# Kernel optimization log

Hardware: AMD Instinct MI355X
Metric: run time of the kernel (lower is better)

## Reference

```python
import jax, jax.numpy as jnp
import numpy as np
from functools import partial

V, H, B, T, L = 32000, 1024, 64, 64, 4
EOS = 2


def setup_inputs() -> dict:
    key = jax.random.key(0)
    ks = jax.random.split(key, 10)
    s = 1.0 / np.sqrt(H)
    return {
        "max_len": T,
        "tgt": jax.random.randint(ks[0], (B, T), 0, V),
        "h0": jax.random.normal(ks[1], (L, B, H), jnp.float32),
        "c0": jax.random.normal(ks[2], (L, B, H), jnp.float32),
        "embedding": jax.random.normal(ks[3], (V, H), jnp.float32) * s,
        "W_ih": jax.random.normal(ks[4], (L, 4 * H, H), jnp.float32) * s,
        "W_hh": jax.random.normal(ks[5], (L, 4 * H, H), jnp.float32) * s,
        "b_ih": jax.random.normal(ks[6], (L, 4 * H), jnp.float32) * s,
        "b_hh": jax.random.normal(ks[7], (L, 4 * H), jnp.float32) * s,
        "W_cls": jax.random.normal(ks[8], (V, H), jnp.float32) * s,
        "b_cls": jax.random.normal(ks[9], (V,), jnp.float32) * s,
    }


def _lstm_cell(x, h, c, Wi, Wh, bi, bh):
    # gates: [B, 4H] in torch order (i, f, g, o)
    g = x @ Wi.T + bi + h @ Wh.T + bh
    i, f, gg, o = jnp.split(g, 4, axis=-1)
    c2 = jax.nn.sigmoid(f) * c + jax.nn.sigmoid(i) * jnp.tanh(gg)
    h2 = jax.nn.sigmoid(o) * jnp.tanh(c2)
    return h2, c2


def reference(max_len, tgt, h0, c0, embedding, W_ih, W_hh, b_ih, b_hh, W_cls, b_cls):
    # step i>0 uses embedding of tgt[:, i-1].
    batch = tgt.shape[0]
    x0 = jnp.broadcast_to(embedding[EOS], (batch, embedding.shape[1]))
    tf_in = embedding[tgt[:, : max_len - 1]]              # [B, T-1, H]
    inputs = jnp.concatenate([x0[:, None, :], tf_in], axis=1)  # [B, T, H]
    inputs = jnp.swapaxes(inputs, 0, 1)                   # [T, B, H]

    def step(carry, x):
        h, c = carry  # each [L, B, H]
        hs, cs = [], []
        inp = x
        for l in range(L):  # 4 stacked LSTM cells, h of cell l feeds cell l+1
            hn, cn = _lstm_cell(inp, h[l], c[l], W_ih[l], W_hh[l], b_ih[l], b_hh[l])
            hs.append(hn)
            cs.append(cn)
            inp = hn
        h = jnp.stack(hs)
        c = jnp.stack(cs)
        logp = jax.nn.log_softmax(h[L - 1] @ W_cls.T + b_cls, axis=-1)  # [B, V]
        return (h, c), logp

    (h, c), out = jax.lax.scan(step, (h0, c0), inputs)
    return out, h, c  # out: [T, B, V]
```

## Files before the change

kernel.cpp:

```cpp
#include <hip/hip_runtime.h>

using u16 = unsigned short;
using u32 = unsigned int;

typedef __bf16 bf16x8 __attribute__((ext_vector_type(8)));
typedef float  f32x4  __attribute__((ext_vector_type(4)));
typedef u16    u16x8  __attribute__((ext_vector_type(8)));

static constexpr int kV = 32000, kH = 1024, kB = 64, kT = 64, kL = 4, kEOS = 2;

struct Flag { int v; int pad[15]; };

__device__ __forceinline__ u16 f2bf(float f) {
  u32 u = __float_as_uint(f);
  u = (u + 0x7fffu + ((u >> 16) & 1u)) >> 16;
  return (u16)u;
}
__device__ __forceinline__ float sigf(float x)   { return 1.0f / (1.0f + __expf(-x)); }
__device__ __forceinline__ float tanhf_(float x) { return 1.0f - 2.0f / (__expf(2.0f * x) + 1.0f); }

typedef const __attribute__((address_space(1))) u32* gas_ptr;
typedef __attribute__((address_space(3))) u32*       las_ptr;
__device__ __forceinline__ void async16(const u16* g, u16* l) {
  __builtin_amdgcn_global_load_lds((gas_ptr)g, (las_ptr)l, 16, 0, 0);
}

__device__ __forceinline__ void spin_ge(const int* p, int tgt) {
  while (__hip_atomic_load(p, __ATOMIC_RELAXED, __HIP_MEMORY_SCOPE_AGENT) < tgt)
    __builtin_amdgcn_s_sleep(2);
}

__device__ __forceinline__ size_t packed_off(int b, int k) {
  return (size_t)(((b >> 4) * 32 + (k >> 5)) * 512 + (((k >> 3) & 3) * 16 + (b & 15)) * 8 + (k & 7));
}

__device__ __forceinline__ u16x8 cvt8(const float* src) {
  const float4* s4 = (const float4*)src;
  float4 v0 = s4[0], v1 = s4[1];
  u16x8 r;
  r[0]=f2bf(v0.x); r[1]=f2bf(v0.y); r[2]=f2bf(v0.z); r[3]=f2bf(v0.w);
  r[4]=f2bf(v1.x); r[5]=f2bf(v1.y); r[6]=f2bf(v1.z); r[7]=f2bf(v1.w);
  return r;
}


__global__ void __launch_bounds__(256)
pack_lstm(const float* __restrict__ Wih, const float* __restrict__ Whh,
          u16* __restrict__ wpack) {
  __shared__ u16 lds[64 * 136];
  const int bid = blockIdx.x;
  const int lblk = bid >> 4, mt = (bid >> 3) & 1, kkg = bid & 7;
  const int lay = lblk >> 6, cb = lblk & 63;
  const int tid = threadIdx.x;
  const float* W = mt ? Whh : Wih;
  {
    const int rid = tid >> 2, q = tid & 3;
    const int gr = (rid >> 4) * 1024 + cb * 16 + (rid & 15);
    const float* src = W + ((size_t)lay * 4096 + gr) * 1024 + kkg * 128 + q * 32;
    u16* dst = lds + rid * 136 + q * 32;
    #pragma unroll
    for (int it = 0; it < 4; ++it)
      *(u16x8*)(dst + it * 8) = cvt8(src + it * 8);
  }
  __syncthreads();
  const int cf = tid >> 6, lane = tid & 63;
  const int rid = cf * 16 + (lane & 15);
  const int l4o = (lane >> 4) * 8;
  #pragma unroll
  for (int kl = 0; kl < 4; ++kl) {
    const int kk = kkg * 4 + kl;
    const u16x8 v = *(const u16x8*)(lds + rid * 136 + kl * 32 + l4o);
    *(u16x8*)(wpack + ((size_t)lblk * 16384 + mt * 8192 + kk * 256 + cf * 64 + lane) * 8) = v;
  }
}

__global__ void __launch_bounds__(256)
pack_cls(const float* __restrict__ W, u16* __restrict__ o) {
  __shared__ u16 lds[128 * 136];
  const int bid = blockIdx.x;
  const int bn = bid >> 3, kkg = bid & 7;
  const int tid = threadIdx.x;
  {
    const int row = tid >> 1, half = tid & 1;
    const float* src = W + ((size_t)(bn * 128 + row)) * 1024 + kkg * 128 + half * 64;
    u16* dst = lds + row * 136 + half * 64;
    #pragma unroll
    for (int it = 0; it < 8; ++it)
      *(u16x8*)(dst + it * 8) = cvt8(src + it * 8);
  }
  __syncthreads();
  #pragma unroll
  for (int kl = 0; kl < 4; ++kl) {
    const int kk = kkg * 4 + kl;
    #pragma unroll
    for (int q = 0; q < 2; ++q) {
      const int p = tid + q * 256, row = p & 127, l4 = p >> 7;
      const u16x8 v = *(const u16x8*)(lds + row * 136 + kl * 32 + l4 * 8);
      *(u16x8*)(o + ((size_t)bn * 16384 + kk * 512 + p) * 8) = v;
    }
  }
}

__global__ void pack_x(const float* __restrict__ emb, const int* __restrict__ tgt,
                       u16* __restrict__ X) {
  const int cid = blockIdx.x * 256 + threadIdx.x;
  const int kc = cid & 127, b = (cid >> 7) & 63, t = cid >> 13;
  const int tok = (t == 0) ? kEOS : tgt[b * 64 + t - 1];
  const u16x8 r = cvt8(emb + (size_t)tok * 1024 + kc * 8);
  *(u16x8*)(X + (size_t)t * 65536 + packed_off(b, kc * 8)) = r;
}

__global__ void pack_init(const float* __restrict__ h0, const float* __restrict__ bih,
                          const float* __restrict__ bhh, u16* __restrict__ hball,
                          float* __restrict__ bsum) {
  const int cid = blockIdx.x * 256 + threadIdx.x;
  if (cid < 32768) {
    const int kc = cid & 127, row = cid >> 7;
    const int lay = row >> 6, b = row & 63;
    const u16x8 r = cvt8(h0 + (size_t)cid * 8);
    *(u16x8*)(hball + (size_t)lay * 65 * 65536 + packed_off(b, kc * 8)) = r;
  } else {
    const int i = cid - 32768;
    bsum[i] = bih[i] + bhh[i];
  }
}

__global__ void __launch_bounds__(1024, 4)
lstm_coop(const u16* __restrict__ wpack, const u16* __restrict__ xall,
          u16* __restrict__ hball, const float* __restrict__ bsum,
          const float* __restrict__ c0, float* __restrict__ outh, float* __restrict__ outc,
          Flag* flags) {
  __shared__ u16 stg[3][32][512];
  __shared__ float Gc[2][64][80];

  const int tid = threadIdx.x, lane = tid & 63, wave = tid >> 6;
  const int l15 = lane & 15, l4 = lane >> 4;
  const int cmat = wave >> 3, cwc = (wave >> 1) & 3, ckh = wave & 1;
  const int blk = blockIdx.x;
  const int lay = (blk >> 1) & 3;
  const int cb  = ((blk >> 3) << 1) | (blk & 1);
  const int u0 = cb << 4;
  const int ub = tid >> 4, uu = tid & 15;

  float creg = c0[((size_t)lay * 64 + ub) * 1024 + u0 + uu];
  float bsv[4];
  #pragma unroll
  for (int g = 0; g < 4; ++g) bsv[g] = bsum[lay * 4096 + g * 1024 + u0 + uu];

  const size_t wbase = (size_t)(lay * 64 + cb) * 131072;
  bf16x8 breg[16];
  #pragma unroll
  for (int j = 0; j < 16; ++j)
    breg[j] = *(const bf16x8*)(wpack + wbase
        + (size_t)(((cmat * 32 + 2 * j + ckh) * 4) + cwc) * 512 + lane * 8);

  const int j0 = wave * 2, j1 = wave * 2 + 1;
  const int m2a = j0 >> 4, mta = (j0 >> 2) & 3, ksla = j0 & 3;
  const int m2b = j1 >> 4, mtb = (j1 >> 2) & 3, kslb = j1 & 3;

  u16* hlay = hball + (size_t)lay * 65 * 65536;
  const u16* hprev = (lay == 0) ? xall : (hball + (size_t)(lay - 1) * 65 * 65536);

  #pragma unroll 1
  for (int t = 0; t < kT; ++t) {
    if (t > 0 && tid < 64)                 spin_ge(&flags[lay * 64 + tid].v, t);
    if (lay > 0 && tid >= 64 && tid < 128) spin_ge(&flags[(lay - 1) * 64 + (tid - 64)].v, t + 1);
    __syncthreads();

    const u16* xsrc = (lay == 0) ? (xall + (size_t)t * 65536)
                                 : (hprev + (size_t)(t + 1) * 65536);
    const u16* hsrc = hlay + (size_t)t * 65536;

    const u16* ga = (m2a ? hsrc : xsrc) + (size_t)((mta * 32 + ksla) * 512) + lane * 8;
    const u16* gb = (m2b ? hsrc : xsrc) + (size_t)((mtb * 32 + kslb) * 512) + lane * 8;

    auto STAGE = [&](int c) {
      async16(ga + (size_t)c * 2048, &stg[c % 3][m2a * 16 + mta * 4 + ksla][0]);
      async16(gb + (size_t)c * 2048, &stg[c % 3][m2b * 16 + mtb * 4 + kslb][0]);
    };

    f32x4 acc[4] = {};
    STAGE(0); STAGE(1);
    #pragma unroll
    for (int c = 0; c < 8; ++c) {
      if (c < 7) asm volatile("s_waitcnt vmcnt(2)" ::: "memory");
      else       asm volatile("s_waitcnt vmcnt(0)" ::: "memory");
      __builtin_amdgcn_s_barrier();
      asm volatile("" ::: "memory");
      if (c < 6) STAGE(c + 2);
      const u16* As = &stg[c % 3][cmat * 16][0];
      #pragma unroll
      for (int s = 0; s < 2; ++s) {
        const int ksl = 2 * s + ckh;
        bf16x8 a[4];
        #pragma unroll
        for (int m = 0; m < 4; ++m)
          a[m] = *(const bf16x8*)(As + (m * 4 + ksl) * 512 + lane * 8);
        #pragma unroll
        for (int m = 0; m < 4; ++m)
          acc[m] = __builtin_amdgcn_mfma_f32_16x16x32_bf16(a[m], breg[2 * c + s], acc[m], 0, 0, 0);
      }
    }

    if (ckh == 0) {
      #pragma unroll
      for (int m = 0; m < 4; ++m)
        #pragma unroll
        for (int r = 0; r < 4; ++r)
          Gc[cmat][m * 16 + l4 * 4 + r][cwc * 16 + l15] = acc[m][r];
    }
    __syncthreads();
    if (ckh == 1) {
      #pragma unroll
      for (int m = 0; m < 4; ++m)
        #pragma unroll
        for (int r = 0; r < 4; ++r)
          Gc[cmat][m * 16 + l4 * 4 + r][cwc * 16 + l15] += acc[m][r];
    }
    __syncthreads();

    float sg[4];
    #pragma unroll
    for (int g = 0; g < 4; ++g) {
      const int col = g * 16 + uu;
      sg[g] = Gc[0][ub][col] + Gc[1][ub][col] + bsv[g];
    }
    const float c2 = sigf(sg[1]) * creg + sigf(sg[0]) * tanhf_(sg[2]);
    const float h2 = sigf(sg[3]) * tanhf_(c2);
    creg = c2;
    const u16 hv = f2bf(h2);
    if (t == kT - 1) {
      outh[((size_t)lay * 64 + ub) * 1024 + u0 + uu] = h2;
      outc[((size_t)lay * 64 + ub) * 1024 + u0 + uu] = c2;
    }
    const u32 other = __shfl_xor((u32)hv, 1);
    if ((tid & 1) == 0) {
      const u32 hpair = (u32)hv | (other << 16);
      u32* hdst = (u32*)(hlay + (size_t)(t + 1) * 65536 + packed_off(ub, u0 + uu));
      __hip_atomic_store(hdst, hpair, __ATOMIC_RELAXED, __HIP_MEMORY_SCOPE_AGENT);
    }
    __syncthreads();
    if (tid == 0)
      __hip_atomic_store(&flags[lay * 64 + cb].v, t + 1, __ATOMIC_RELAXED, __HIP_MEMORY_SCOPE_AGENT);
  }
}

#define CLS_EPILOGUE()                                                                     \
  {                                                                                        \
    float* sRm = (float*)&sA[0][0];                                          \
    float* sRs = sRm + 256;                                                                \
    _Pragma("unroll")                                                                      \
    for (int mi = 0; mi < 4; ++mi) {                                                       \
      _Pragma("unroll")                                                                    \
      for (int r = 0; r < 4; ++r) {                                                        \
        float v[4];                                                                        \
        _Pragma("unroll")                                                                  \
        for (int ci = 0; ci < 4; ++ci) v[ci] = acc[mi][ci][r] + bc[ci];                     \
        float mx = fmaxf(fmaxf(v[0], v[1]), fmaxf(v[2], v[3]));                            \
        mx = fmaxf(mx, __shfl_xor(mx, 1)); mx = fmaxf(mx, __shfl_xor(mx, 2));              \
        mx = fmaxf(mx, __shfl_xor(mx, 4)); mx = fmaxf(mx, __shfl_xor(mx, 8));              \
        float ss = __expf(v[0]-mx) + __expf(v[1]-mx) + __expf(v[2]-mx) + __expf(v[3]-mx);  \
        ss += __shfl_xor(ss, 1); ss += __shfl_xor(ss, 2);                                  \
        ss += __shfl_xor(ss, 4); ss += __shfl_xor(ss, 8);                                  \
        const int lr = wm * 64 + mi * 16 + l4 * 4 + r;                                     \
        if (l15 == 0) { sRm[wc * 128 + lr] = mx; sRs[wc * 128 + lr] = ss; }                \
      }                                                                                    \
    }                                                                                      \
    __syncthreads();                                                                       \
    if (tid < 128) {                                                                       \
      const float m0 = sRm[tid], s0 = sRs[tid];                                            \
      const float m1 = sRm[128 + tid], s1 = sRs[128 + tid];                                \
      const float M = fmaxf(m0, m1);                                                       \
      const float S = s0 * __expf(m0 - M) + s1 * __expf(m1 - M);                           \
      pmax[(size_t)(bm * 128 + tid) * 256 + bn] = M;                                       \
      psum[(size_t)(bm * 128 + tid) * 256 + bn] = S;                                       \
    }                                                                                      \
  }

__global__ void __launch_bounds__(256)
cls_gemm(const u16* __restrict__ A, const u16* __restrict__ Bw,
         const float* __restrict__ bcls, float* __restrict__ out,
         float* __restrict__ pmax, float* __restrict__ psum) {
  __shared__ u16 sA[3][4096], sB[3][4096];
  const int tid = threadIdx.x, lane = tid & 63, wave = tid >> 6;
  const int wm = wave >> 1, wc = wave & 1;
  const int l15 = lane & 15, l4 = lane >> 4;
  const int bm = blockIdx.x, bn = blockIdx.y;
  const u16* Ab = A  + (size_t)bm * 131072;
  const u16* Bb = Bw + (size_t)bn * 131072;

  auto STAGE = [&](int kk) {
    u16* dA = sA[kk % 3]; u16* dB = sB[kk % 3];
    #pragma unroll
    for (int q = 0; q < 4; ++q) {
      const int u = wave * 4 + q;
      if (u < 8) {
        const u16* g = Ab + (size_t)(u >> 2) * 65536 + (size_t)(((u & 3) * 32 + kk) * 512) + lane * 8;
        async16(g, dA + u * 512);
      } else {
        const int v = u & 7;
        const u16* g = Bb + (size_t)kk * 4096 + v * 512 + lane * 8;
        async16(g, dB + v * 512);
      }
    }
  };

  f32x4 acc[4][4] = {};
  STAGE(0); STAGE(1);
  for (int kk = 0; kk < 32; ++kk) {
    if (kk < 31) asm volatile("s_waitcnt vmcnt(4)" ::: "memory");
    else         asm volatile("s_waitcnt vmcnt(0)" ::: "memory");
    __builtin_amdgcn_s_barrier();
    asm volatile("" ::: "memory");
    if (kk < 30) STAGE(kk + 2);
    const u16* aS = sA[kk % 3]; const u16* bS = sB[kk % 3];
    bf16x8 av[4], bv[4];
    #pragma unroll
    for (int mi = 0; mi < 4; ++mi) av[mi] = *(const bf16x8*)(aS + (wm * 4 + mi) * 512 + lane * 8);
    #pragma unroll
    for (int ci = 0; ci < 4; ++ci) bv[ci] = *(const bf16x8*)(bS + l4 * 1024 + (wc * 64 + ci * 16 + l15) * 8);
    #pragma unroll
    for (int mi = 0; mi < 4; ++mi)
      #pragma unroll
      for (int ci = 0; ci < 4; ++ci)
        acc[mi][ci] = __builtin_amdgcn_mfma_f32_16x16x32_bf16(av[mi], bv[ci], acc[mi][ci], 0, 0, 0);
  }
  float bc[4];
  #pragma unroll
  for (int ci = 0; ci < 4; ++ci) bc[ci] = bcls[bn * 128 + wc * 64 + ci * 16 + l15];
  #pragma unroll
  for (int ci = 0; ci < 4; ++ci) {
    const int col = bn * 128 + wc * 64 + ci * 16 + l15;
    #pragma unroll
    for (int mi = 0; mi < 4; ++mi)
      #pragma unroll
      for (int r = 0; r < 4; ++r) {
        const int row = bm * 128 + wm * 64 + mi * 16 + l4 * 4 + r;
        out[(size_t)row * 32000 + col] = acc[mi][ci][r] + bc[ci];
      }
  }
  __syncthreads();
  CLS_EPILOGUE()
}

__global__ void __launch_bounds__(256)
cls_gemm_f32(const u16* __restrict__ A, const float* __restrict__ Bw,
             const float* __restrict__ bcls, float* __restrict__ out,
             float* __restrict__ pmax, float* __restrict__ psum) {
  __shared__ u16 sA[3][4096], sB[3][4096];
  const int tid = threadIdx.x, lane = tid & 63, wave = tid >> 6;
  const int wm = wave >> 1, wc = wave & 1;
  const int l15 = lane & 15, l4 = lane >> 4;
  const int bm = blockIdx.x, bn = blockIdx.y;
  const u16*  Ab = A  + (size_t)bm * 131072;
  const float* Bb = Bw + (size_t)bn * 131072;

  auto LOADB = [&](int kk, u16x8* rb) {
    #pragma unroll
    for (int q = 0; q < 2; ++q) {
      const int p = tid + q * 256, row = p & 127, khi = p >> 7;
      rb[q] = cvt8(Bb + (size_t)row * 1024 + kk * 32 + khi * 8);
    }
  };
  auto WRITEB = [&](int kk, const u16x8* rb) {
    u16* dB = sB[kk % 3];
    #pragma unroll
    for (int q = 0; q < 2; ++q) {
      const int p = tid + q * 256, row = p & 127, khi = p >> 7;
      *(u16x8*)(dB + khi * 1024 + row * 8) = rb[q];
    }
  };
  auto STAGE_A = [&](int kk) {
    u16* dA = sA[kk % 3];
    #pragma unroll
    for (int q = 0; q < 2; ++q) {
      const int v = wave * 2 + q;
      const u16* g = Ab + (size_t)(v >> 2) * 65536 + (size_t)(((v & 3) * 32 + kk) * 512) + lane * 8;
      async16(g, dA + v * 512);
    }
  };

  f32x4 acc[4][4] = {};
  {
    u16x8 rb[2];
    LOADB(0, rb); STAGE_A(0); WRITEB(0, rb);
  }
  for (int kk = 0; kk < 32; ++kk) {
    if (kk < 31) {
      u16x8 rb[2];
      LOADB(kk + 1, rb);
      STAGE_A(kk + 1);
      WRITEB(kk + 1, rb);
    } else {
      asm volatile("s_waitcnt vmcnt(0)" ::: "memory");
    }
    __builtin_amdgcn_s_barrier();
    asm volatile("" ::: "memory");
    const u16* aS = sA[kk % 3]; const u16* bS = sB[kk % 3];
    bf16x8 av[4], bv[4];
    #pragma unroll
    for (int mi = 0; mi < 4; ++mi) av[mi] = *(const bf16x8*)(aS + (wm * 4 + mi) * 512 + lane * 8);
    #pragma unroll
    for (int ci = 0; ci < 4; ++ci) bv[ci] = *(const bf16x8*)(bS + l4 * 1024 + (wc * 64 + ci * 16 + l15) * 8);
    #pragma unroll
    for (int mi = 0; mi < 4; ++mi)
      #pragma unroll
      for (int ci = 0; ci < 4; ++ci)
        acc[mi][ci] = __builtin_amdgcn_mfma_f32_16x16x32_bf16(av[mi], bv[ci], acc[mi][ci], 0, 0, 0);
    asm volatile("" ::: "memory");
    __builtin_amdgcn_s_barrier();
  }
  float bc[4];
  #pragma unroll
  for (int ci = 0; ci < 4; ++ci) bc[ci] = bcls[bn * 128 + wc * 64 + ci * 16 + l15];
  #pragma unroll
  for (int ci = 0; ci < 4; ++ci) {
    const int col = bn * 128 + wc * 64 + ci * 16 + l15;
    #pragma unroll
    for (int mi = 0; mi < 4; ++mi)
      #pragma unroll
      for (int r = 0; r < 4; ++r) {
        const int row = bm * 128 + wm * 64 + mi * 16 + l4 * 4 + r;
        out[(size_t)row * 32000 + col] = acc[mi][ci][r] + bc[ci];
      }
  }
  __syncthreads();
  CLS_EPILOGUE()
}

__global__ void __launch_bounds__(256)
lsm_sub(const float* __restrict__ pmax, const float* __restrict__ psum,
        float* __restrict__ out) {
  __shared__ float rm[256], rs[256];
  const int r = blockIdx.x, b = threadIdx.x;
  float m = -3.0e38f, s = 0.0f;
  if (b < 250) { m = pmax[(size_t)r * 256 + b]; s = psum[(size_t)r * 256 + b]; }
  rm[b] = m; rs[b] = s; __syncthreads();
  for (int st = 128; st > 0; st >>= 1) {
    if (b < st) {
      const float m2 = rm[b + st], s2 = rs[b + st];
      const float M = fmaxf(rm[b], m2);
      rs[b] = rs[b] * __expf(rm[b] - M) + s2 * __expf(m2 - M);
      rm[b] = M;
    }
    __syncthreads();
  }
  const float z = rm[0] + logf(rs[0]);
  float4* p = (float4*)(out + (size_t)r * 32000);
  for (int v = b; v < 8000; v += 256) {
    float4 x = p[v];
    x.x -= z; x.y -= z; x.z -= z; x.w -= z;
    p[v] = x;
  }
}

extern "C" void kernel_launch(void* const* d_in, const int* in_sizes, int n_in,
                              void* d_out, int out_size, void* d_ws, size_t ws_size,
                              hipStream_t stream) {
  (void)in_sizes; (void)n_in; (void)out_size;
  const int*   tgt  = (const int*)d_in[1];
  const float* h0   = (const float*)d_in[2];
  const float* c0   = (const float*)d_in[3];
  const float* emb  = (const float*)d_in[4];
  const float* Wih  = (const float*)d_in[5];
  const float* Whh  = (const float*)d_in[6];
  const float* bih  = (const float*)d_in[7];
  const float* bhh  = (const float*)d_in[8];
  const float* Wcls = (const float*)d_in[9];
  const float* bcls = (const float*)d_in[10];

  float* out  = (float*)d_out;
  float* outh = out + (size_t)kT * kB * kV;
  float* outc = outh + (size_t)kL * kB * kH;

  const size_t SZ_WPACK = 67108864;
  const size_t SZ_WCLS  = 65536000;
  const size_t SZ_X     = 8388608;
  const size_t SZ_HBALL = 34078720;
  const size_t SZ_BSUM  = 65536;
  const size_t SZ_FLAGS = 16384;
  const size_t SZ_PM    = 4194304;
  const size_t FULL_REQ = SZ_WPACK + SZ_WCLS + SZ_X + SZ_HBALL + SZ_BSUM + SZ_FLAGS + 2 * SZ_PM;
  const bool full = (ws_size >= FULL_REQ);

  char* ws = (char*)d_ws;
  size_t off = 0;
  u16* wpack = (u16*)(ws + off); off += SZ_WPACK;
  u16* wclsb = nullptr;
  if (full) { wclsb = (u16*)(ws + off); off += SZ_WCLS; }
  u16*   X     = (u16*)(ws + off); off += SZ_X;
  u16*   hball = (u16*)(ws + off); off += SZ_HBALL;
  float* bsum  = (float*)(ws + off); off += SZ_BSUM;
  Flag*  flags = (Flag*)(ws + off);  off += SZ_FLAGS;
  float* pmax  = (float*)(ws + off); off += SZ_PM;
  float* psum  = (float*)(ws + off); off += SZ_PM;

  pack_lstm<<<4096, 256, 0, stream>>>(Wih, Whh, wpack);
  if (full) pack_cls<<<2000, 256, 0, stream>>>(Wcls, wclsb);
  pack_x   <<<2048,  256, 0, stream>>>(emb, tgt, X);
  pack_init<<<192,   256, 0, stream>>>(h0, bih, bhh, hball, bsum);
  hipMemsetAsync(flags, 0, SZ_FLAGS, stream);

  void* args[] = { (void*)&wpack, (void*)&X, (void*)&hball, (void*)&bsum,
                   (void*)&c0, (void*)&outh, (void*)&outc, (void*)&flags };
  hipLaunchCooperativeKernel((const void*)lstm_coop, dim3(256), dim3(1024), args, 0, stream);

  const u16* h3a = hball + (size_t)3 * 65 * 65536 + 65536;
  if (full) cls_gemm    <<<dim3(32, 250), 256, 0, stream>>>(h3a, wclsb, bcls, out, pmax, psum);
  else      cls_gemm_f32<<<dim3(32, 250), 256, 0, stream>>>(h3a, Wcls,  bcls, out, pmax, psum);
  lsm_sub<<<4096, 256, 0, stream>>>(pmax, psum, out);
}
```

Measured before the change: 1.243 ms.

## Widen classifier GEMM tile to 128x256 with 8 waves and raise MFMA priority

The bf16 classifier GEMM now uses 512-thread blocks that each compute a 128x256 output tile covering two vocab panels, so every A tile staged into LDS is reused across twice as many columns and the grid halves to 32x125. The softmax partial epilogue is adapted to emit per-panel max and sum for both panels. Separately, the LSTM recurrent kernel raises wave priority around its MFMA inner loop. The larger tile uses more LDS per block and fewer blocks, which may reduce occupancy or latency hiding.

```diff
diff --git a/kernel.cpp b/kernel.cpp
--- a/kernel.cpp
+++ b/kernel.cpp
@@ -189,6 +189,7 @@
       asm volatile("" ::: "memory");
       if (c < 6) STAGE(c + 2);
       const u16* As = &stg[c % 3][cmat * 16][0];
+      __builtin_amdgcn_s_setprio(1);
       #pragma unroll
       for (int s = 0; s < 2; ++s) {
         const int ksl = 2 * s + ckh;
@@ -200,6 +201,7 @@
         for (int m = 0; m < 4; ++m)
           acc[m] = __builtin_amdgcn_mfma_f32_16x16x32_bf16(a[m], breg[2 * c + s], acc[m], 0, 0, 0);
       }
+      __builtin_amdgcn_s_setprio(0);
     }
 
     if (ckh == 0) {
@@ -245,9 +247,107 @@
   }
 }
 
-#define CLS_EPILOGUE()                                                                     \
+__global__ void __launch_bounds__(512, 4)
+cls_gemm(const u16* __restrict__ A, const u16* __restrict__ Bw,
+         const float* __restrict__ bcls, float* __restrict__ out,
+         float* __restrict__ pmax, float* __restrict__ psum) {
+  __shared__ u16 sA[3][4096], sB[3][8192];
+  const int tid = threadIdx.x, lane = tid & 63, wave = tid >> 6;
+  const int wm = wave >> 2, wc = wave & 3;
+  const int l15 = lane & 15, l4 = lane >> 4;
+  const int bm = blockIdx.x, bny = blockIdx.y;
+  const int bn0 = bny * 2;
+  const u16* Ab = A + (size_t)bm * 131072;
+
+  auto STAGE = [&](int kk) {
+    u16* dA = sA[kk % 3]; u16* dB = sB[kk % 3];
+    #pragma unroll
+    for (int q = 0; q < 3; ++q) {
+      const int c = wave * 3 + q;
+      if (c < 8) {
+        const u16* g = Ab + (size_t)(c >> 2) * 65536 + (size_t)(((c & 3) * 32 + kk) * 512) + lane * 8;
+        async16(g, dA + c * 512);
+      } else {
+        const int b = c - 8, pan = b >> 3, v = b & 7;
+        const u16* g = Bw + (size_t)(bn0 + pan) * 131072 + (size_t)kk * 4096 + v * 512 + lane * 8;
+        async16(g, dB + pan * 4096 + v * 512);
+      }
+    }
+  };
+
+  f32x4 acc[4][4] = {};
+  STAGE(0); STAGE(1);
+  for (int kk = 0; kk < 32; ++kk) {
+    if (kk < 31) asm volatile("s_waitcnt vmcnt(3)" ::: "memory");
+    else         asm volatile("s_waitcnt vmcnt(0)" ::: "memory");
+    __builtin_amdgcn_s_barrier();
+    asm volatile("" ::: "memory");
+    if (kk < 30) STAGE(kk + 2);
+    const u16* aS = sA[kk % 3]; const u16* bS = sB[kk % 3];
+    const int pan = wc >> 1, cbase = (wc & 1) * 64;
+    bf16x8 av[4], bv[4];
+    #pragma unroll
+    for (int mi = 0; mi < 4; ++mi) av[mi] = *(const bf16x8*)(aS + (wm * 4 + mi) * 512 + lane * 8);
+    #pragma unroll
+    for (int ci = 0; ci < 4; ++ci)
+      bv[ci] = *(const bf16x8*)(bS + pan * 4096 + l4 * 1024 + (cbase + ci * 16 + l15) * 8);
+    #pragma unroll
+    for (int mi = 0; mi < 4; ++mi)
+      #pragma unroll
+      for (int ci = 0; ci < 4; ++ci)
+        acc[mi][ci] = __builtin_amdgcn_mfma_f32_16x16x32_bf16(av[mi], bv[ci], acc[mi][ci], 0, 0, 0);
+  }
+  float bc[4];
+  #pragma unroll
+  for (int ci = 0; ci < 4; ++ci) bc[ci] = bcls[bn0 * 128 + wc * 64 + ci * 16 + l15];
+  #pragma unroll
+  for (int ci = 0; ci < 4; ++ci) {
+    const int col = bn0 * 128 + wc * 64 + ci * 16 + l15;
+    #pragma unroll
+    for (int mi = 0; mi < 4; ++mi)
+      #pragma unroll
+      for (int r = 0; r < 4; ++r) {
+        const int row = bm * 128 + wm * 64 + mi * 16 + l4 * 4 + r;
+        out[(size_t)row * 32000 + col] = acc[mi][ci][r] + bc[ci];
+      }
+  }
+  __syncthreads();
+  {
+    float* sRm = (float*)&sA[0][0];
+    float* sRs = sRm + 512;
+    #pragma unroll
+    for (int mi = 0; mi < 4; ++mi) {
+      #pragma unroll
+      for (int r = 0; r < 4; ++r) {
+        float v[4];
+        #pragma unroll
+        for (int ci = 0; ci < 4; ++ci) v[ci] = acc[mi][ci][r] + bc[ci];
+        float mx = fmaxf(fmaxf(v[0], v[1]), fmaxf(v[2], v[3]));
+        mx = fmaxf(mx, __shfl_xor(mx, 1)); mx = fmaxf(mx, __shfl_xor(mx, 2));
+        mx = fmaxf(mx, __shfl_xor(mx, 4)); mx = fmaxf(mx, __shfl_xor(mx, 8));
+        float ss = __expf(v[0]-mx) + __expf(v[1]-mx) + __expf(v[2]-mx) + __expf(v[3]-mx);
+        ss += __shfl_xor(ss, 1); ss += __shfl_xor(ss, 2);
+        ss += __shfl_xor(ss, 4); ss += __shfl_xor(ss, 8);
+        const int lr = wm * 64 + mi * 16 + l4 * 4 + r;
+        if (l15 == 0) { sRm[wc * 128 + lr] = mx; sRs[wc * 128 + lr] = ss; }
+      }
+    }
+    __syncthreads();
+    if (tid < 256) {
+      const int pan = tid >> 7, row = tid & 127;
+      const float m0 = sRm[(pan * 2) * 128 + row],     s0 = sRs[(pan * 2) * 128 + row];
+      const float m1 = sRm[(pan * 2 + 1) * 128 + row], s1 = sRs[(pan * 2 + 1) * 128 + row];
+      const float M = fmaxf(m0, m1);
+      const float S = s0 * __expf(m0 - M) + s1 * __expf(m1 - M);
+      pmax[(size_t)(bm * 128 + row) * 256 + (bn0 + pan)] = M;
+      psum[(size_t)(bm * 128 + row) * 256 + (bn0 + pan)] = S;
+    }
+  }
+}
+
+#define CLS_EPILOGUE_128()                                                                 \
   {                                                                                        \
-    float* sRm = (float*)&sA[0][0];                                          \
+    float* sRm = (float*)&sA[0][0];                                                        \
     float* sRs = sRm + 256;                                                                \
     _Pragma("unroll")                                                                      \
     for (int mi = 0; mi < 4; ++mi) {                                                       \
@@ -278,72 +378,6 @@
   }
 
 __global__ void __launch_bounds__(256)
-cls_gemm(const u16* __restrict__ A, const u16* __restrict__ Bw,
-         const float* __restrict__ bcls, float* __restrict__ out,
-         float* __restrict__ pmax, float* __restrict__ psum) {
-  __shared__ u16 sA[3][4096], sB[3][4096];
-  const int tid = threadIdx.x, lane = tid & 63, wave = tid >> 6;
-  const int wm = wave >> 1, wc = wave & 1;
-  const int l15 = lane & 15, l4 = lane >> 4;
-  const int bm = blockIdx.x, bn = blockIdx.y;
-  const u16* Ab = A  + (size_t)bm * 131072;
-  const u16* Bb = Bw + (size_t)bn * 131072;
-
-  auto STAGE = [&](int kk) {
-    u16* dA = sA[kk % 3]; u16* dB = sB[kk % 3];
-    #pragma unroll
-    for (int q = 0; q < 4; ++q) {
-      const int u = wave * 4 + q;
-      if (u < 8) {
-        const u16* g = Ab + (size_t)(u >> 2) * 65536 + (size_t)(((u & 3) * 32 + kk) * 512) + lane * 8;
-        async16(g, dA + u * 512);
-      } else {
-        const int v = u & 7;
-        const u16* g = Bb + (size_t)kk * 4096 + v * 512 + lane * 8;
-        async16(g, dB + v * 512);
-      }
-    }
-  };
-
-  f32x4 acc[4][4] = {};
-  STAGE(0); STAGE(1);
-  for (int kk = 0; kk < 32; ++kk) {
-    if (kk < 31) asm volatile("s_waitcnt vmcnt(4)" ::: "memory");
-    else         asm volatile("s_waitcnt vmcnt(0)" ::: "memory");
-    __builtin_amdgcn_s_barrier();
-    asm volatile("" ::: "memory");
-    if (kk < 30) STAGE(kk + 2);
-    const u16* aS = sA[kk % 3]; const u16* bS = sB[kk % 3];
-    bf16x8 av[4], bv[4];
-    #pragma unroll
-    for (int mi = 0; mi < 4; ++mi) av[mi] = *(const bf16x8*)(aS + (wm * 4 + mi) * 512 + lane * 8);
-    #pragma unroll
-    for (int ci = 0; ci < 4; ++ci) bv[ci] = *(const bf16x8*)(bS + l4 * 1024 + (wc * 64 + ci * 16 + l15) * 8);
-    #pragma unroll
-    for (int mi = 0; mi < 4; ++mi)
-      #pragma unroll
-      for (int ci = 0; ci < 4; ++ci)
-        acc[mi][ci] = __builtin_amdgcn_mfma_f32_16x16x32_bf16(av[mi], bv[ci], acc[mi][ci], 0, 0, 0);
-  }
-  float bc[4];
-  #pragma unroll
-  for (int ci = 0; ci < 4; ++ci) bc[ci] = bcls[bn * 128 + wc * 64 + ci * 16 + l15];
-  #pragma unroll
-  for (int ci = 0; ci < 4; ++ci) {
-    const int col = bn * 128 + wc * 64 + ci * 16 + l15;
-    #pragma unroll
-    for (int mi = 0; mi < 4; ++mi)
-      #pragma unroll
-      for (int r = 0; r < 4; ++r) {
-        const int row = bm * 128 + wm * 64 + mi * 16 + l4 * 4 + r;
-        out[(size_t)row * 32000 + col] = acc[mi][ci][r] + bc[ci];
-      }
-  }
-  __syncthreads();
-  CLS_EPILOGUE()
-}
-
-__global__ void __launch_bounds__(256)
 cls_gemm_f32(const u16* __restrict__ A, const float* __restrict__ Bw,
              const float* __restrict__ bcls, float* __restrict__ out,
              float* __restrict__ pmax, float* __restrict__ psum) {
@@ -425,7 +459,7 @@
       }
   }
   __syncthreads();
-  CLS_EPILOGUE()
+  CLS_EPILOGUE_128()
 }
 
 __global__ void __launch_bounds__(256)
@@ -506,7 +540,7 @@
   hipLaunchCooperativeKernel((const void*)lstm_coop, dim3(256), dim3(1024), args, 0, stream);
 
   const u16* h3a = hball + (size_t)3 * 65 * 65536 + 65536;
-  if (full) cls_gemm    <<<dim3(32, 250), 256, 0, stream>>>(h3a, wclsb, bcls, out, pmax, psum);
+  if (full) cls_gemm    <<<dim3(32, 125), 512, 0, stream>>>(h3a, wclsb, bcls, out, pmax, psum);
   else      cls_gemm_f32<<<dim3(32, 250), 256, 0, stream>>>(h3a, Wcls,  bcls, out, pmax, psum);
   lsm_sub<<<4096, 256, 0, stream>>>(pmax, psum, out);
 }
```

New measurement: 1.246 ms. About the same (+0.2%).
